# Optimization experiments

Measured on AMD Instinct MI355X. Metric: run time of the kernel, lower is better.

Reference implementation:

```python
import jax, jax.numpy as jnp
import numpy as np

KH, KW = 3, 3
PAD = (1, 1, 1, 1)  # torch F.pad order: (W_left, W_right, H_top, H_bottom)
STRIDE = 1
B, CIN, COUT, H, W = 4, 32, 32, 128, 128


def setup_inputs() -> dict:
    key = jax.random.key(0)
    k1, k2, k3, k4 = jax.random.split(key, 4)
    f = jax.random.normal(k1, (B, CIN, H, W), jnp.float32)
    # orientation field components (cos/sin of a random angle field)
    theta = jax.random.uniform(k2, (B, CIN, H, W), jnp.float32, 0.0, 2.0 * np.pi)
    r0 = jnp.cos(theta)
    r1 = jnp.sin(theta)
    # learned conv weight (nn.Conv2d default uniform init, no bias)
    fan_in = CIN * KH * KW
    bound = 1.0 / np.sqrt(fan_in)
    w = jax.random.uniform(k3, (COUT, CIN, KH, KW), jnp.float32, -bound, bound)
    # frozen wr: (randn * pi * 100) / a with a = 100  ->  randn * pi
    wr = jax.random.normal(k4, (COUT, CIN, KH, KW), jnp.float32) * np.pi
    return {"f": f, "r0": r0, "r1": r1, "w": w, "wr": wr}


def _rot90(w):
    # torch: w.permute(0,1,2,4,3).flip([4]) on the (kh,kw) dims
    return jnp.flip(jnp.swapaxes(w, -1, -2), -1)


def _conv_single(f, r0, r1, w, wr):
    # f, r0, r1: (B, Cin, Hp, Wp);  w, wr: (Cout, Cin, KH, KW)
    Hp, Wp = f.shape[2], f.shape[3]
    he = Hp - PAD[0] - PAD[1]
    we = Wp - PAD[2] - PAD[3]
    s = STRIDE
    out = None
    for i in range(KH):
        for j in range(KW):
            fw = f[:, :, i:i + he:s, j:j + we:s]    # (B, Cin, h, w)
            r0w = r0[:, :, i:i + he:s, j:j + we:s]
            r1w = r1[:, :, i:i + he:s, j:j + we:s]
            c = jnp.cos(wr[:, :, i, j])[None, :, :, None, None]   # (1, Cout, Cin, 1, 1)
            sn = jnp.sin(wr[:, :, i, j])[None, :, :, None, None]
            # lambda_theta: relu of orientation-projected field, (B, Cout, Cin, h, w)
            lam = jax.nn.relu(c * r0w[:, None] + sn * r1w[:, None])
            term = jnp.einsum('bchw,oc,bochw->bohw', fw, w[:, :, i, j], lam)
            out = term if out is None else out + term
    return out  # (B, Cout, h, w)


def _forward(f, r0, r1, w, wr):
    pl, pr, pt, pb = PAD
    pad = ((0, 0), (0, 0), (pt, pb), (pl, pr))
    fp = jnp.pad(f, pad)
    r0p = jnp.pad(r0, pad)
    r1p = jnp.pad(r1, pad)
    orient = jnp.arange(4, dtype=f.dtype) * jnp.asarray(np.pi / 2, f.dtype)
    outs = []
    wk = w
    for o in range(4):
        if o > 0:
            wk = _rot90(wk)
        outs.append(_conv_single(fp, r0p, r1p, wk, wr + orient[o]))
    stacked = jnp.stack(outs, axis=2)              # (B, Cout, 4, h, w)
    idx = jnp.argmax(stacked, axis=2)              # (B, Cout, h, w)
    out = jnp.take_along_axis(stacked, idx[:, :, None], axis=2)[:, :, 0]
    out_r = orient[idx]                            # winning orientation angle
    return out, jnp.cos(out_r), jnp.sin(out_r)


def reference(f, r0, r1, w, wr):
    return _forward(f, r0, r1, w, wr)
```

## Files before the change

kernel.cpp:

```cpp
#include <hip/hip_runtime.h>


typedef float v2f __attribute__((ext_vector_type(2)));

#define B_    4
#define CIN_  32
#define COUT_ 32
#define H_    128
#define W_    128
#define HW_   (H_ * W_)
#define OUTSZ_ (B_ * COUT_ * H_ * W_)

__global__ __launch_bounds__(256)
void build_wtab(const float* __restrict__ w, const float* __restrict__ wr,
                float* __restrict__ tab)
{
    int idx = blockIdx.x * 256 + threadIdx.x;
    if (idx >= CIN_ * 9 * COUT_) return;
    int oc  = idx & 31;
    int t2  = idx >> 5;
    int tap = t2 % 9;
    int cc  = t2 / 9;
    int i = tap / 3, j = tap - i * 3;
    int base = (oc * CIN_ + cc) * 9;
    float w0 = w[base + i * 3 + j];
    float w1 = w[base + (2 - j) * 3 + i];
    float w2 = w[base + (2 - i) * 3 + (2 - j)];
    float w3 = w[base + j * 3 + (2 - i)];
    float S, C;
    sincosf(wr[base + i * 3 + j], &S, &C);
    float* dst = tab + (size_t)idx * 8;
    dst[0] = C;  dst[1] = S;
    dst[2] = w0; dst[3] = w1;
    dst[4] = w2; dst[5] = w3;
    dst[6] = 0.0f; dst[7] = 0.0f;
}

#define NC_    8
#define NG_    (CIN_ / NC_)
#define ROWF_  68
#define CLSTR_ (3 * ROWF_)
#define USED_  (NC_ * CLSTR_)
#define PLANE_ 1636

struct WRow { float4 a0, a1, a2; float2 b0, b1, b2; };

#define LOAD_WROW(Wd) do {                                                  \
    const float* _wp = wanchor + soff;                                      \
    (Wd).a0 = *reinterpret_cast<const float4*>(_wp - 256);                  \
    (Wd).b0 = *reinterpret_cast<const float2*>(_wp - 252);                  \
    (Wd).a1 = *reinterpret_cast<const float4*>(_wp);                        \
    (Wd).b1 = *reinterpret_cast<const float2*>(_wp + 4);                    \
    (Wd).a2 = *reinterpret_cast<const float4*>(_wp + 256);                  \
    (Wd).b2 = *reinterpret_cast<const float2*>(_wp + 260);                  \
    soff += 768;                                                            \
    soff = (soff < 72960) ? soff : 72960;    \
    __builtin_amdgcn_sched_group_barrier(0x020, 6, 0);    \
} while (0)

#define CORE_TAP(W4, W2, JJ) do {                                           \
    v2f _C2  = {(W4).x, (W4).x};                                            \
    v2f _S2  = {(W4).y, (W4).y};                                            \
    v2f _w0  = {(W4).z, (W4).z};                                            \
    v2f _w1  = {(W4).w, (W4).w};                                            \
    v2f _w2  = {(W2).x, (W2).x};                                            \
    v2f _w3  = {(W2).y, (W2).y};                                            \
    _Pragma("unroll")                                                       \
    for (int _q = 0; _q < 2; ++_q) {                                        \
        v2f _f  = _fP[_q + (JJ)];                                           \
        v2f _r0 = _aP[_q + (JJ)];                                           \
        v2f _r1 = _bP[_q + (JJ)];                                           \
        v2f _m1 = _S2 * _r1;                                                \
        v2f _u  = __builtin_elementwise_fma(_C2, _r0, _m1);                 \
        v2f _m2 = _S2 * _r0;                                                \
        v2f _vv = __builtin_elementwise_fma(_C2, _r1, -_m2);                \
        v2f _g0 = __builtin_elementwise_max(_u,  (v2f)(0.0f));              \
        v2f _g1 = __builtin_elementwise_max(_vv, (v2f)(0.0f));              \
        v2f _t0 = _f * _g0;                                                 \
        v2f _t1 = _f * _g1;                                                 \
        v2f _t2 = __builtin_elementwise_fma(_f, -_u,  _t0);                 \
        v2f _t3 = __builtin_elementwise_fma(_f, -_vv, _t1);                 \
        acc[_q][0] = __builtin_elementwise_fma(_t0, _w0, acc[_q][0]);       \
        acc[_q][1] = __builtin_elementwise_fma(_t1, _w1, acc[_q][1]);       \
        acc[_q][2] = __builtin_elementwise_fma(_t2, _w2, acc[_q][2]);       \
        acc[_q][3] = __builtin_elementwise_fma(_t3, _w3, acc[_q][3]);       \
    }                                                                       \
} while (0)

#define COMPUTE_ROW(Wr, CL, II) do {                                        \
    const int _bi = (CL) * CLSTR_ + (II) * ROWF_ + (p << 1);                \
    float4 _fA = *reinterpret_cast<const float4*>(&sm[_bi]);                \
    float4 _fB = *reinterpret_cast<const float4*>(&sm[_bi + 4]);            \
    float4 _aA = *reinterpret_cast<const float4*>(&sm[PLANE_ + _bi]);       \
    float4 _aB = *reinterpret_cast<const float4*>(&sm[PLANE_ + _bi + 4]);   \
    float4 _bA = *reinterpret_cast<const float4*>(&sm[2 * PLANE_ + _bi]);   \
    float4 _bB = *reinterpret_cast<const float4*>(&sm[2 * PLANE_ + _bi + 4]);\
    v2f _fP[4] = {{_fA.x,_fA.y},{_fA.z,_fA.w},{_fB.x,_fB.y},{_fB.z,_fB.w}}; \
    v2f _aP[4] = {{_aA.x,_aA.y},{_aA.z,_aA.w},{_aB.x,_aB.y},{_aB.z,_aB.w}}; \
    v2f _bP[4] = {{_bA.x,_bA.y},{_bA.z,_bA.w},{_bB.x,_bB.y},{_bB.z,_bB.w}}; \
    CORE_TAP((Wr).a0, (Wr).b0, 0);                                          \
    CORE_TAP((Wr).a1, (Wr).b1, 1);                                          \
    CORE_TAP((Wr).a2, (Wr).b2, 2);                                          \
} while (0)

#define STEP(WLD, WUSE, CL, II) do {                                        \
    LOAD_WROW(WLD);                                                         \
    COMPUTE_ROW(WUSE, CL, II);                                              \
} while (0)

__global__ __launch_bounds__(512, 3)
void orient_conv_kernel(const float* __restrict__ f,
                        const float* __restrict__ r0,
                        const float* __restrict__ r1,
                        const float* __restrict__ tab,
                        float* __restrict__ out)
{
    __shared__ float sm[3 * PLANE_];

    const int tid   = threadIdx.x;
    const int oc    = tid & 31;
    const int pxg   = tid >> 5;
    const int p     = pxg << 1;
    const int bid   = blockIdx.x;
    const int b     = bid >> 8;
    const int rem   = bid & 255;
    const int h     = rem >> 1;
    const int wbase = (rem & 1) << 6;

    int      goff[4], sidx[4];
    unsigned msk[4];
#pragma unroll
    for (int k = 0; k < 4; ++k) {
        int s = tid + (k << 9);
        if (s < USED_) {
            int cl  = s / CLSTR_;
            int r2  = s - cl * CLSTR_;
            int row = r2 / ROWF_;
            int q2  = r2 - row * ROWF_;
            int col = (q2 >> 1) + ((q2 & 1) << 5);
            int gh = h + row - 1;
            int gw = wbase + col - 1;
            bool ok = ((unsigned)gh < (unsigned)H_) & ((unsigned)gw < (unsigned)W_);
            goff[k] = ok ? (cl * HW_ + gh * W_ + gw) : 0;
            msk[k]  = ok ? 0xFFFFFFFFu : 0u;
            sidx[k] = s;
        } else { goff[k] = 0; msk[k] = 0u; sidx[k] = USED_; }
    }
    const bool have3 = (tid + 1536) < USED_;
    const int chanBase = b * (CIN_ * HW_);

    v2f acc[2][4];
#pragma unroll
    for (int q = 0; q < 2; ++q)
#pragma unroll
        for (int o = 0; o < 4; ++o) acc[q][o] = (v2f)(0.0f);

    const float* wanchor = tab + (size_t)((1 << 5) | oc) * 8;
    int soff = 0;
    WRow WA, WB;
    LOAD_WROW(WA);

    float tF[4], tA[4], tB[4];
    {
        const float* fb = f  + chanBase;
        const float* ab = r0 + chanBase;
        const float* bb = r1 + chanBase;
#pragma unroll
        for (int k = 0; k < 3; ++k) {
            tF[k] = fb[goff[k]]; tA[k] = ab[goff[k]]; tB[k] = bb[goff[k]];
        }
        if (have3) { tF[3] = fb[goff[3]]; tA[3] = ab[goff[3]]; tB[3] = bb[goff[3]]; }
    }

#pragma unroll 1
    for (int g = 0; g < NG_; ++g) {
        __syncthreads();
#pragma unroll
        for (int k = 0; k < 3; ++k) {
            sm[             sidx[k]] = __uint_as_float(__float_as_uint(tF[k]) & msk[k]);
            sm[PLANE_     + sidx[k]] = __uint_as_float(__float_as_uint(tA[k]) & msk[k]);
            sm[2 * PLANE_ + sidx[k]] = __uint_as_float(__float_as_uint(tB[k]) & msk[k]);
        }
        if (have3) {
            sm[             sidx[3]] = __uint_as_float(__float_as_uint(tF[3]) & msk[3]);
            sm[PLANE_     + sidx[3]] = __uint_as_float(__float_as_uint(tA[3]) & msk[3]);
            sm[2 * PLANE_ + sidx[3]] = __uint_as_float(__float_as_uint(tB[3]) & msk[3]);
        }
        __syncthreads();

        if (g + 1 < NG_) {
            const int gb = chanBase + (g + 1) * (NC_ * HW_);
            const float* fb = f  + gb;
            const float* ab = r0 + gb;
            const float* bb = r1 + gb;
#pragma unroll
            for (int k = 0; k < 3; ++k) {
                tF[k] = fb[goff[k]]; tA[k] = ab[goff[k]]; tB[k] = bb[goff[k]];
            }
            if (have3) { tF[3] = fb[goff[3]]; tA[3] = ab[goff[3]]; tB[3] = bb[goff[3]]; }
        }

#pragma unroll 1
        for (int cl = 0; cl < NC_; cl += 2) {
            STEP(WB, WA, cl,     0);
            STEP(WA, WB, cl,     1);
            STEP(WB, WA, cl,     2);
            STEP(WA, WB, cl + 1, 0);
            STEP(WB, WA, cl + 1, 1);
            STEP(WA, WB, cl + 1, 2);
        }
    }

    const float cosv[4] = {1.0f, -4.37113883e-08f, -1.0f, 1.19248806e-08f};
    const float sinv[4] = {0.0f, 1.0f, -8.74227766e-08f, -1.0f};
#pragma unroll
    for (int q = 0; q < 2; ++q) {
#pragma unroll
        for (int k = 0; k < 2; ++k) {
            int wcol = wbase + p + q + (k << 5);
            float a0 = acc[q][0][k], a1 = acc[q][1][k];
            float a2 = acc[q][2][k], a3 = acc[q][3][k];
            float best = a0; int bi = 0;
            if (a1 > best) { best = a1; bi = 1; }
            if (a2 > best) { best = a2; bi = 2; }
            if (a3 > best) { best = a3; bi = 3; }
            size_t o = ((size_t)(b * COUT_ + oc) * H_ + h) * W_ + wcol;
            out[o]              = best;
            out[o + OUTSZ_]     = cosv[bi];
            out[o + 2 * OUTSZ_] = sinv[bi];
        }
    }
}

extern "C" void kernel_launch(void* const* d_in, const int* in_sizes, int n_in,
                              void* d_out, int out_size, void* d_ws, size_t ws_size,
                              hipStream_t stream)
{
    const float* f  = (const float*)d_in[0];
    const float* r0 = (const float*)d_in[1];
    const float* r1 = (const float*)d_in[2];
    const float* w  = (const float*)d_in[3];
    const float* wr = (const float*)d_in[4];
    float* out = (float*)d_out;
    float* tab = (float*)d_ws;

    build_wtab<<<dim3(36), dim3(256), 0, stream>>>(w, wr, tab);
    orient_conv_kernel<<<dim3(B_ * H_ * 2), dim3(512), 0, stream>>>(
        f, r0, r1, tab, out);
}
```

Baseline: 270.3 us.

## Double-buffer LDS input tiles and remap block IDs across XCDs

Moves from one shared-memory buffer to two. The next channel group is written into the alternate buffer after compute, and the group after that is prefetched, so each iteration needs one barrier instead of two. Block indices are also permuted so that consecutive block IDs map to spread-out work, likely to improve L2 locality across XCDs. LDS use doubles to about 39 KB per block, which may limit occupancy under the 3-blocks-per-CU launch bound.

```diff
diff --git a/kernel.cpp b/kernel.cpp
--- a/kernel.cpp
+++ b/kernel.cpp
@@ -42,6 +42,7 @@
 #define CLSTR_ (3 * ROWF_)
 #define USED_  (NC_ * CLSTR_)
 #define PLANE_ 1636
+#define NBUF_  (3 * PLANE_)
 
 struct WRow { float4 a0, a1, a2; float2 b0, b1, b2; };
 
@@ -87,14 +88,15 @@
     }                                                                       \
 } while (0)
 
-#define COMPUTE_ROW(Wr, CL, II) do {                                        \
+#define COMPUTE_ROW(Wr, RB, CL, II) do {                                    \
+    const float* _rb = (RB);                                                \
     const int _bi = (CL) * CLSTR_ + (II) * ROWF_ + (p << 1);                \
-    float4 _fA = *reinterpret_cast<const float4*>(&sm[_bi]);                \
-    float4 _fB = *reinterpret_cast<const float4*>(&sm[_bi + 4]);            \
-    float4 _aA = *reinterpret_cast<const float4*>(&sm[PLANE_ + _bi]);       \
-    float4 _aB = *reinterpret_cast<const float4*>(&sm[PLANE_ + _bi + 4]);   \
-    float4 _bA = *reinterpret_cast<const float4*>(&sm[2 * PLANE_ + _bi]);   \
-    float4 _bB = *reinterpret_cast<const float4*>(&sm[2 * PLANE_ + _bi + 4]);\
+    float4 _fA = *reinterpret_cast<const float4*>(&_rb[_bi]);               \
+    float4 _fB = *reinterpret_cast<const float4*>(&_rb[_bi + 4]);           \
+    float4 _aA = *reinterpret_cast<const float4*>(&_rb[PLANE_ + _bi]);      \
+    float4 _aB = *reinterpret_cast<const float4*>(&_rb[PLANE_ + _bi + 4]);  \
+    float4 _bA = *reinterpret_cast<const float4*>(&_rb[2 * PLANE_ + _bi]);  \
+    float4 _bB = *reinterpret_cast<const float4*>(&_rb[2 * PLANE_ + _bi + 4]);\
     v2f _fP[4] = {{_fA.x,_fA.y},{_fA.z,_fA.w},{_fB.x,_fB.y},{_fB.z,_fB.w}}; \
     v2f _aP[4] = {{_aA.x,_aA.y},{_aA.z,_aA.w},{_aB.x,_aB.y},{_aB.z,_aB.w}}; \
     v2f _bP[4] = {{_bA.x,_bA.y},{_bA.z,_bA.w},{_bB.x,_bB.y},{_bB.z,_bB.w}}; \
@@ -103,9 +105,36 @@
     CORE_TAP((Wr).a2, (Wr).b2, 2);                                          \
 } while (0)
 
-#define STEP(WLD, WUSE, CL, II) do {                                        \
+#define STEP(WLD, WUSE, RB, CL, II) do {                                    \
     LOAD_WROW(WLD);                                                         \
-    COMPUTE_ROW(WUSE, CL, II);                                              \
+    COMPUTE_ROW(WUSE, RB, CL, II);                                          \
+} while (0)
+
+#define STAGE_LOAD(GI) do {                                                 \
+    const int _gb = chanBase + (GI) * (NC_ * HW_);                          \
+    const float* _fb = f  + _gb;                                            \
+    const float* _ab = r0 + _gb;                                            \
+    const float* _bb = r1 + _gb;                                            \
+    _Pragma("unroll")                                                       \
+    for (int _k = 0; _k < 3; ++_k) {                                        \
+        tF[_k] = _fb[goff[_k]]; tA[_k] = _ab[goff[_k]]; tB[_k] = _bb[goff[_k]]; \
+    }                                                                       \
+    if (have3) { tF[3] = _fb[goff[3]]; tA[3] = _ab[goff[3]]; tB[3] = _bb[goff[3]]; } \
+} while (0)
+
+#define STAGE_WRITE(DST) do {                                               \
+    float* _d = (DST);                                                      \
+    _Pragma("unroll")                                                       \
+    for (int _k = 0; _k < 3; ++_k) {                                        \
+        _d[             sidx[_k]] = __uint_as_float(__float_as_uint(tF[_k]) & msk[_k]); \
+        _d[PLANE_     + sidx[_k]] = __uint_as_float(__float_as_uint(tA[_k]) & msk[_k]); \
+        _d[2 * PLANE_ + sidx[_k]] = __uint_as_float(__float_as_uint(tB[_k]) & msk[_k]); \
+    }                                                                       \
+    if (have3) {                                                            \
+        _d[             sidx[3]] = __uint_as_float(__float_as_uint(tF[3]) & msk[3]); \
+        _d[PLANE_     + sidx[3]] = __uint_as_float(__float_as_uint(tA[3]) & msk[3]); \
+        _d[2 * PLANE_ + sidx[3]] = __uint_as_float(__float_as_uint(tB[3]) & msk[3]); \
+    }                                                                       \
 } while (0)
 
 __global__ __launch_bounds__(512, 3)
@@ -115,13 +144,14 @@
                         const float* __restrict__ tab,
                         float* __restrict__ out)
 {
-    __shared__ float sm[3 * PLANE_];
+    __shared__ float sm[2 * NBUF_];
 
     const int tid   = threadIdx.x;
     const int oc    = tid & 31;
     const int pxg   = tid >> 5;
     const int p     = pxg << 1;
-    const int bid   = blockIdx.x;
+    const int obid  = blockIdx.x;
+    const int bid   = (obid & 7) * ((B_ * H_ * 2) >> 3) + (obid >> 3);
     const int b     = bid >> 8;
     const int rem   = bid & 255;
     const int h     = rem >> 1;
@@ -161,53 +191,30 @@
     LOAD_WROW(WA);
 
     float tF[4], tA[4], tB[4];
-    {
-        const float* fb = f  + chanBase;
-        const float* ab = r0 + chanBase;
-        const float* bb = r1 + chanBase;
-#pragma unroll
-        for (int k = 0; k < 3; ++k) {
-            tF[k] = fb[goff[k]]; tA[k] = ab[goff[k]]; tB[k] = bb[goff[k]];
-        }
-        if (have3) { tF[3] = fb[goff[3]]; tA[3] = ab[goff[3]]; tB[3] = bb[goff[3]]; }
-    }
+    STAGE_LOAD(0);
+    STAGE_WRITE(sm);
+    STAGE_LOAD(1);
+    __syncthreads();
 
 #pragma unroll 1
     for (int g = 0; g < NG_; ++g) {
-        __syncthreads();
-#pragma unroll
-        for (int k = 0; k < 3; ++k) {
-            sm[             sidx[k]] = __uint_as_float(__float_as_uint(tF[k]) & msk[k]);
-            sm[PLANE_     + sidx[k]] = __uint_as_float(__float_as_uint(tA[k]) & msk[k]);
-            sm[2 * PLANE_ + sidx[k]] = __uint_as_float(__float_as_uint(tB[k]) & msk[k]);
-        }
-        if (have3) {
-            sm[             sidx[3]] = __uint_as_float(__float_as_uint(tF[3]) & msk[3]);
-            sm[PLANE_     + sidx[3]] = __uint_as_float(__float_as_uint(tA[3]) & msk[3]);
-            sm[2 * PLANE_ + sidx[3]] = __uint_as_float(__float_as_uint(tB[3]) & msk[3]);
-        }
-        __syncthreads();
-
-        if (g + 1 < NG_) {
-            const int gb = chanBase + (g + 1) * (NC_ * HW_);
-            const float* fb = f  + gb;
-            const float* ab = r0 + gb;
-            const float* bb = r1 + gb;
-#pragma unroll
-            for (int k = 0; k < 3; ++k) {
-                tF[k] = fb[goff[k]]; tA[k] = ab[goff[k]]; tB[k] = bb[goff[k]];
-            }
-            if (have3) { tF[3] = fb[goff[3]]; tA[3] = ab[goff[3]]; tB[3] = bb[goff[3]]; }
-        }
+        const float* rb = sm + (g & 1) * NBUF_;
 
 #pragma unroll 1
         for (int cl = 0; cl < NC_; cl += 2) {
-            STEP(WB, WA, cl,     0);
-            STEP(WA, WB, cl,     1);
-            STEP(WB, WA, cl,     2);
-            STEP(WA, WB, cl + 1, 0);
-            STEP(WB, WA, cl + 1, 1);
-            STEP(WA, WB, cl + 1, 2);
+            STEP(WB, WA, rb, cl,     0);
+            STEP(WA, WB, rb, cl,     1);
+            STEP(WB, WA, rb, cl,     2);
+            STEP(WA, WB, rb, cl + 1, 0);
+            STEP(WB, WA, rb, cl + 1, 1);
+            STEP(WA, WB, rb, cl + 1, 2);
+        }
+
+        if (g + 1 < NG_) {
+            float* wbuf = sm + ((g + 1) & 1) * NBUF_;
+            STAGE_WRITE(wbuf);
+            if (g + 2 < NG_) STAGE_LOAD(g + 2);
+            __syncthreads();
         }
     }
 
```

New measurement: 267.7 us, median of 2. No clear change (-1.0%).
